# Performance work log

Hardware: AMD Instinct MI355X
Metric: run time of the kernel (lower is better)

Reference implementation:

```python
import jax, jax.numpy as jnp
import numpy as np

CH = 32          # channels
HID = CH * 16    # GRU hidden/input size = 512


def setup_inputs() -> dict:
    key = jax.random.key(0)
    ks = jax.random.split(key, 9)
    B, T = 512, 128
    s = 1.0 / np.sqrt(HID)
    frames = jax.random.uniform(ks[0], (B, T, 1, 16, 16), dtype=jnp.float32)
    conv_w = jax.random.normal(ks[1], (CH, 2, 4, 4), jnp.float32) * 0.1
    conv_b = jax.random.normal(ks[2], (CH,), jnp.float32) * 0.01
    w_ih = jax.random.uniform(ks[3], (3 * HID, HID), jnp.float32, -s, s)
    w_hh = jax.random.uniform(ks[4], (3 * HID, HID), jnp.float32, -s, s)
    b_ih = jax.random.uniform(ks[5], (3 * HID,), jnp.float32, -s, s)
    b_hh = jax.random.uniform(ks[6], (3 * HID,), jnp.float32, -s, s)
    deconv_w = jax.random.normal(ks[7], (CH, 1, 4, 4), jnp.float32) * 0.1
    deconv_b = jax.random.normal(ks[8], (1,), jnp.float32) * 0.01
    return {"frames": frames, "conv_w": conv_w, "conv_b": conv_b,
            "w_ih": w_ih, "w_hh": w_hh, "b_ih": b_ih, "b_hh": b_hh,
            "deconv_w": deconv_w, "deconv_b": deconv_b}


def reference(frames, conv_w, conv_b, w_ih, w_hh, b_ih, b_hh, deconv_w, deconv_b):
    B, T = frames.shape[0], frames.shape[1]
    T2 = T - 2
    curr = frames[:, 1:T - 1]              # (B,T2,1,16,16)
    prev = frames[:, :T - 2]               # (B,T2,1,16,16)
    diff = jnp.concatenate([curr, prev], axis=2)  # (B,T2,2,16,16)

    # Encoder: Conv2d(2,CH,4,stride=4). Stride==kernel -> non-overlapping patches.
    # Reshape HxW=16x16 into (i,p,j,q) with H=4i+p, W=4j+q.
    x = diff.reshape(B * T2, 2, 4, 4, 4, 4)                 # (n,c,i,p,j,q)
    enc = jnp.einsum('bcipjq,ocpq->boij', x, conv_w) + conv_b[None, :, None, None]
    feat = jax.nn.gelu(enc, approximate=False).reshape(B, T2, HID)  # flatten(1), exact GELU

    # GRU (single layer, batch_first, zero init hidden)
    gates_x = jnp.einsum('bti,gi->tbg', feat, w_ih) + b_ih  # (T2,B,3H)

    def step(h, gx):
        gh = h @ w_hh.T + b_hh
        gxr, gxz, gxn = jnp.split(gx, 3, axis=-1)
        ghr, ghz, ghn = jnp.split(gh, 3, axis=-1)
        r = jax.nn.sigmoid(gxr + ghr)
        z = jax.nn.sigmoid(gxz + ghz)
        n = jnp.tanh(gxn + r * ghn)
        h_new = (1.0 - z) * n + z * h
        return h_new, h_new

    h0 = jnp.zeros((B, HID), frames.dtype)
    _, outs = jax.lax.scan(step, h0, gates_x)               # (T2,B,HID)

    # Decoder: ConvTranspose2d(CH,1,4,stride=4). Stride==kernel -> scatter patches.
    dec_in = outs.transpose(1, 0, 2).reshape(B * T2, CH, 4, 4)
    dec = jnp.einsum('ncij,copq->noipjq', dec_in, deconv_w).reshape(B * T2, 1, 16, 16)
    delta = jnp.tanh(dec + deconv_b[None, :, None, None])

    pred = jnp.clip(curr.reshape(B * T2, 1, 16, 16) + delta, 0.0, 1.0)
    return pred.reshape(B, T2, 1, 16, 16)
```

## Files before the change

kernel.cpp:

```cpp
#include <hip/hip_runtime.h>
#include <cstdint>

typedef float f32x4 __attribute__((ext_vector_type(4)));
typedef __bf16 bf16x8 __attribute__((ext_vector_type(8)));
typedef unsigned short us8 __attribute__((ext_vector_type(8)));
typedef unsigned int u32x4 __attribute__((ext_vector_type(4)));

#define T2 126

__device__ __forceinline__ unsigned short f2bf(float x){
  union { float f; uint32_t u; } v; v.f = x;
  return (unsigned short)((v.u + 0x7fffu + ((v.u >> 16) & 1u)) >> 16);
}
__device__ __forceinline__ float bf2f(unsigned short h){
  union { uint32_t u; float f; } v; v.u = ((uint32_t)h) << 16; return v.f;
}
__device__ __forceinline__ f32x4 mfma_bf16(us8 a, us8 b, f32x4 c){
  return __builtin_amdgcn_mfma_f32_16x16x32_bf16(
      __builtin_bit_cast(bf16x8, a), __builtin_bit_cast(bf16x8, b), c, 0, 0, 0);
}
__device__ __forceinline__ float sigm(float x){ return 1.0f / (1.0f + __expf(-x)); }

#define HSWZ(row, chunk) ((row) * 512 + ((((chunk) ^ ((row) & 7))) << 3))

__global__ void __launch_bounds__(256) pack_w_kernel(const float* __restrict__ w,
                                                     unsigned short* __restrict__ dst){
  int tid = blockIdx.x * 256 + threadIdx.x;
  int l = tid & 63;
  int tile = tid >> 6;
  int kt = tile & 15, jt = tile >> 4;
  int row = jt * 16 + (l & 15);
  int col = kt * 32 + (l >> 4) * 8;
  const float* s = w + (size_t)row * 512 + col;
  unsigned short o[8];
  #pragma unroll
  for (int e = 0; e < 8; e++) o[e] = f2bf(s[e]);
  *(us8*)(dst + (size_t)tid * 8) = *(const us8*)o;
}

__global__ void __launch_bounds__(256) conv_gelu_kernel(const float* __restrict__ frames,
                                                        const float* __restrict__ cw,
                                                        const float* __restrict__ cb,
                                                        unsigned short* __restrict__ featg){
  __shared__ float im[512];
  __shared__ float wl[1024];
  int n = blockIdx.x;
  int t = n >> 9, b = n & 511;
  const float* fr = frames + ((size_t)b * 128 + t) * 256;
  int tid = threadIdx.x;
  ((float2*)im)[tid] = ((const float2*)fr)[tid];
  #pragma unroll
  for (int i = 0; i < 4; i++) wl[tid + 256 * i] = cw[tid + 256 * i];
  __syncthreads();
  #pragma unroll
  for (int half = 0; half < 2; half++){
    int oi = tid + half * 256;
    int o = oi >> 4, ii = (oi >> 2) & 3, jj = oi & 3;
    const float* wc = &wl[o * 32];
    float s = cb[o];
    #pragma unroll
    for (int p = 0; p < 4; p++)
      #pragma unroll
      for (int q = 0; q < 4; q++){
        int pix = (ii * 4 + p) * 16 + jj * 4 + q;
        s += im[256 + pix] * wc[p * 4 + q] + im[pix] * wc[16 + p * 4 + q];
      }
    float g = 0.5f * s * (1.0f + erff(s * 0.70710678118654752f));
    featg[(size_t)n * 512 + oi] = f2bf(g);
  }
}

__global__ void __launch_bounds__(256) scan_init_kernel(u32x4* __restrict__ hq,
                                                        unsigned int* __restrict__ tagbuf){
  int tid = blockIdx.x * 256 + threadIdx.x;
  int stride = gridDim.x * 256;
  for (int i = tid; i < 32768; i += stride)
    hq[i] = (u32x4){0u, 0u, 0u, 0u};
  for (int i = tid; i < 2 * 8 * 32 * 16; i += stride)
    tagbuf[i] = 0u;
}

__global__ void __launch_bounds__(256, 1) gru_scan_kernel(
    const unsigned short* __restrict__ whh_p,
    const unsigned short* __restrict__ wih_p,
    const float* __restrict__ b_hh,
    const float* __restrict__ b_ih,
    u32x4* __restrict__ hq,
    unsigned int* __restrict__ tagbuf,
    const unsigned short* __restrict__ featg,
    const float* __restrict__ frames,
    const float* __restrict__ dw,
    const float* __restrict__ db,
    float* __restrict__ out){
  __shared__ unsigned short hlds[16 * 512];
  __shared__ unsigned short featl[16 * 512];
  __shared__ unsigned short gbuf[2][3 * 16 * 72];
  __shared__ unsigned short hout[16 * 64];
  __shared__ float dwl[512];
  const int tid = threadIdx.x;
  const int B = blockIdx.x;
  const int grp = B & 31;
  const int slc = B >> 5;
  const int l = tid & 63;
  const int w = tid >> 6;
  const int lr = l & 15, lh = l >> 4;
  const int j = slc * 64 + w * 16 + lr;
  const int rowb = grp * 16;
  const int rloc = lh * 4;

  dwl[tid] = dw[tid]; dwl[tid + 256] = dw[tid + 256];
  const float dbias = db[0];

  us8 wr[16], wz[16], wn[16];
  {
    const int jt = slc * 4 + w;
    #pragma unroll
    for (int kt = 0; kt < 16; kt++){
      wr[kt] = *(volatile const us8*)(whh_p + ((size_t)((jt      ) * 16 + kt) * 512 + l * 8));
      wz[kt] = *(volatile const us8*)(whh_p + ((size_t)((jt + 32) * 16 + kt) * 512 + l * 8));
      wn[kt] = *(volatile const us8*)(whh_p + ((size_t)((jt + 64) * 16 + kt) * 512 + l * 8));
    }
  }
  const float bhr = b_hh[j], bhz = b_hh[512 + j], bhn = b_hh[1024 + j];

  int jtg[3], gg[3], wtt[3]; float gbias[3];
  #pragma unroll
  for (int jj = 0; jj < 3; jj++){
    int q = w * 3 + jj; gg[jj] = q >> 2; wtt[jj] = q & 3;
    jtg[jj] = gg[jj] * 32 + slc * 4 + wtt[jj];
    gbias[jj] = b_ih[gg[jj] * 512 + slc * 64 + wtt[jj] * 16 + lr];
  }
  float hprev[4] = {0.0f, 0.0f, 0.0f, 0.0f};
  __syncthreads();

  auto stagefeat = [&](int u){
    const u32x4* rb = (const u32x4*)(featg + (size_t)u * 512 * 512);
    int quad = tid & 63, r0 = tid >> 6;
    const u32x4* p0 = rb + ((size_t)(rowb + r0) * 64 + quad);
    u32x4 q0 = p0[0];
    u32x4 q1 = p0[4 * 64];
    u32x4 q2 = p0[8 * 64];
    u32x4 q3 = p0[12 * 64];
    *(u32x4*)&featl[HSWZ(r0,      quad)] = q0;
    *(u32x4*)&featl[HSWZ(r0 + 4,  quad)] = q1;
    *(u32x4*)&featl[HSWZ(r0 + 8,  quad)] = q2;
    *(u32x4*)&featl[HSWZ(r0 + 12, quad)] = q3;
    __syncthreads();
  };

  auto gatesgemm = [&](int par){
    f32x4 a0 = {0.f,0.f,0.f,0.f}, a1 = {0.f,0.f,0.f,0.f}, a2 = {0.f,0.f,0.f,0.f};
    #pragma unroll
    for (int kt = 0; kt < 16; kt++){
      us8 a = *(const us8*)&featl[HSWZ(lr, kt * 4 + lh)];
      us8 b0 = *(const us8*)(wih_p + ((size_t)(jtg[0] * 16 + kt) * 512 + l * 8));
      us8 b1 = *(const us8*)(wih_p + ((size_t)(jtg[1] * 16 + kt) * 512 + l * 8));
      us8 b2 = *(const us8*)(wih_p + ((size_t)(jtg[2] * 16 + kt) * 512 + l * 8));
      a0 = mfma_bf16(a, b0, a0);
      a1 = mfma_bf16(a, b1, a1);
      a2 = mfma_bf16(a, b2, a2);
    }
    unsigned short* gb = &gbuf[par][0];
    #pragma unroll
    for (int r = 0; r < 4; r++){
      gb[(gg[0] * 16 + lh * 4 + r) * 72 + wtt[0] * 16 + lr] = f2bf(a0[r] + gbias[0]);
      gb[(gg[1] * 16 + lh * 4 + r) * 72 + wtt[1] * 16 + lr] = f2bf(a1[r] + gbias[1]);
      gb[(gg[2] * 16 + lh * 4 + r) * 72 + wtt[2] * 16 + lr] = f2bf(a2[r] + gbias[2]);
    }
  };

  auto poll = [&](int s){
    if (tid < 8){
      const unsigned int* tp = tagbuf + (((size_t)(s & 1) * 8 + tid) * 32 + grp) * 16;
      unsigned int want = (unsigned)s;
      unsigned int tv;
      for (;;){
        asm volatile("global_load_dword %0, %1, off sc0 sc1\n\ts_waitcnt vmcnt(0)"
                     : "=&v"(tv) : "v"(tp) : "memory");
        if (tv >= want) break;
        __builtin_amdgcn_s_sleep(1);
      }
    }
    __syncthreads();
  };

  auto stage = [&](int s){
    const u32x4* rb = hq + (size_t)(s & 1) * 32768;
    int quad = tid & 63, r0 = tid >> 6;
    const u32x4* p0 = rb + ((size_t)(rowb + r0) * 64 + quad);
    const u32x4* p1 = p0 + 4 * 64;
    const u32x4* p2 = p0 + 8 * 64;
    const u32x4* p3 = p0 + 12 * 64;
    u32x4 q0, q1, q2, q3;
    asm volatile(
      "global_load_dwordx4 %0, %4, off sc0 sc1\n\t"
      "global_load_dwordx4 %1, %5, off sc0 sc1\n\t"
      "global_load_dwordx4 %2, %6, off sc0 sc1\n\t"
      "global_load_dwordx4 %3, %7, off sc0 sc1\n\t"
      "s_waitcnt vmcnt(0)"
      : "=&v"(q0), "=&v"(q1), "=&v"(q2), "=&v"(q3)
      : "v"(p0), "v"(p1), "v"(p2), "v"(p3)
      : "memory");
    *(u32x4*)&hlds[HSWZ(r0,      quad)] = q0;
    *(u32x4*)&hlds[HSWZ(r0 + 4,  quad)] = q1;
    *(u32x4*)&hlds[HSWZ(r0 + 8,  quad)] = q2;
    *(u32x4*)&hlds[HSWZ(r0 + 12, quad)] = q3;
    __syncthreads();
  };

  auto emit = [&](int so){
    int row = tid >> 4;
    int b = rowb + row;
    const float* fr = frames + ((size_t)b * 128 + so + 1) * 256;
    float* ob = out + ((size_t)b * T2 + so) * 256;
    #pragma unroll
    for (int e = 0; e < 2; e++){
      int pi = (tid & 15) * 2 + e;
      int pr = slc * 2 + (pi >> 4), pc = pi & 15;
      int ii = pr >> 2, pp = pr & 3, jj2 = pc >> 2, qq = pc & 3;
      float acc = dbias;
      #pragma unroll
      for (int c = 0; c < 32; c++){
        int ch = c * 16 + ii * 4 + jj2;
        acc += bf2f(hlds[HSWZ(row, ch >> 3) + (ch & 7)]) * dwl[c * 16 + pp * 4 + qq];
      }
      float dlt = tanhf(acc);
      float rv = fr[pr * 16 + pc] + dlt;
      ob[pr * 16 + pc] = fminf(fmaxf(rv, 0.0f), 1.0f);
    }
  };

  stagefeat(0);
  gatesgemm(0);

  for (int s = 0; s < T2; s++){
    if (s + 1 < T2){
      __syncthreads();
      stagefeat(s + 1);
      gatesgemm((s + 1) & 1);
    }
    poll(s);
    stage(s);
    f32x4 aR = {0.f,0.f,0.f,0.f}, aZ = {0.f,0.f,0.f,0.f}, aN = {0.f,0.f,0.f,0.f};
    #pragma unroll
    for (int kt = 0; kt < 16; kt++){
      us8 a = *(const us8*)&hlds[HSWZ(lr, kt * 4 + lh)];
      aR = mfma_bf16(a, wr[kt], aR);
      aZ = mfma_bf16(a, wz[kt], aZ);
      aN = mfma_bf16(a, wn[kt], aN);
    }
    const unsigned short* gb = &gbuf[s & 1][0];
    #pragma unroll
    for (int r = 0; r < 4; r++){
      float gxr = bf2f(gb[(      rloc + r) * 72 + w * 16 + lr]);
      float gxz = bf2f(gb[(16 + rloc + r) * 72 + w * 16 + lr]);
      float gxn = bf2f(gb[(32 + rloc + r) * 72 + w * 16 + lr]);
      float rr = sigm(gxr + aR[r] + bhr);
      float zz = sigm(gxz + aZ[r] + bhz);
      float nn = tanhf(gxn + rr * (aN[r] + bhn));
      float hv = (1.0f - zz) * nn + zz * hprev[r];
      hprev[r] = hv;
      hout[(rloc + r) * 64 + w * 16 + lr] = f2bf(hv);
    }
    __syncthreads();
    if (tid < 128){
      int row = tid >> 3, q = tid & 7;
      u32x4 hv = *(const u32x4*)&hout[row * 64 + q * 8];
      u32x4* dst = hq + ((size_t)(((s + 1) & 1) * 512 + rowb + row) * 64 + slc * 8 + q);
      asm volatile("global_store_dwordx4 %0, %1, off sc0 sc1" :: "v"(dst), "v"(hv) : "memory");
    }
    asm volatile("s_waitcnt vmcnt(0)" ::: "memory");
    __syncthreads();
    if (tid == 0){
      unsigned int tg = (unsigned)(s + 1);
      unsigned int* tp = tagbuf + (((size_t)((s + 1) & 1) * 8 + slc) * 32 + grp) * 16;
      asm volatile("global_store_dword %0, %1, off sc0 sc1" :: "v"(tp), "v"(tg) : "memory");
    }
    if (s >= 1) emit(s - 1);
  }
  poll(T2);
  stage(T2);
  emit(T2 - 1);
}

extern "C" void kernel_launch(void* const* d_in, const int* in_sizes, int n_in,
                              void* d_out, int out_size, void* d_ws, size_t ws_size,
                              hipStream_t stream) {
  const float* frames   = (const float*)d_in[0];
  const float* conv_w   = (const float*)d_in[1];
  const float* conv_b   = (const float*)d_in[2];
  const float* w_ih     = (const float*)d_in[3];
  const float* w_hh     = (const float*)d_in[4];
  const float* b_ih     = (const float*)d_in[5];
  const float* b_hh     = (const float*)d_in[6];
  const float* deconv_w = (const float*)d_in[7];
  const float* deconv_b = (const float*)d_in[8];
  float* out = (float*)d_out;
  char* ws = (char*)d_ws;

  unsigned short* wih_p  = (unsigned short*)(ws);
  unsigned short* whh_p  = (unsigned short*)(ws + 1572864LL);
  u32x4*          hq     = (u32x4*)         (ws + 3145728LL);
  unsigned int*   tagbuf = (unsigned int*)  (ws + 4194304LL);
  unsigned short* featg  = (unsigned short*)(ws + 4227072LL);

  pack_w_kernel<<<384, 256, 0, stream>>>(w_ih, wih_p);
  pack_w_kernel<<<384, 256, 0, stream>>>(w_hh, whh_p);
  scan_init_kernel<<<64, 256, 0, stream>>>(hq, tagbuf);
  conv_gelu_kernel<<<126 * 512, 256, 0, stream>>>(frames, conv_w, conv_b, featg);
  gru_scan_kernel<<<256, 256, 0, stream>>>(whh_p, wih_p, b_hh, b_ih, hq, tagbuf,
                                           featg, frames, deconv_w, deconv_b, out);
}
```

Baseline: 1.010 ms.

## Move next-step feature staging and input GEMM off the recurrence critical path

Feature prefetch and the input-gate GEMM for step s+1 now run after the hidden state for step s is published, not before polling. The feature loads are issued alongside the h store, and a partial vmcnt wait orders the h store before the tag store. This lets the input-side work overlap other blocks' latency in the cross-block recurrence instead of delaying each poll. It relies on careful vmcnt accounting: the wait assumes only the four feature loads may still be outstanding.

Measured after the change: 993.2 us. About the same (-1.7%).

```diff
diff --git a/kernel.cpp b/kernel.cpp
--- a/kernel.cpp
+++ b/kernel.cpp
@@ -133,20 +133,7 @@
   float hprev[4] = {0.0f, 0.0f, 0.0f, 0.0f};
   __syncthreads();
 
-  auto stagefeat = [&](int u){
-    const u32x4* rb = (const u32x4*)(featg + (size_t)u * 512 * 512);
-    int quad = tid & 63, r0 = tid >> 6;
-    const u32x4* p0 = rb + ((size_t)(rowb + r0) * 64 + quad);
-    u32x4 q0 = p0[0];
-    u32x4 q1 = p0[4 * 64];
-    u32x4 q2 = p0[8 * 64];
-    u32x4 q3 = p0[12 * 64];
-    *(u32x4*)&featl[HSWZ(r0,      quad)] = q0;
-    *(u32x4*)&featl[HSWZ(r0 + 4,  quad)] = q1;
-    *(u32x4*)&featl[HSWZ(r0 + 8,  quad)] = q2;
-    *(u32x4*)&featl[HSWZ(r0 + 12, quad)] = q3;
-    __syncthreads();
-  };
+  const int fquad = tid & 63, fr0 = tid >> 6;
 
   auto gatesgemm = [&](int par){
     f32x4 a0 = {0.f,0.f,0.f,0.f}, a1 = {0.f,0.f,0.f,0.f}, a2 = {0.f,0.f,0.f,0.f};
@@ -186,8 +173,7 @@
 
   auto stage = [&](int s){
     const u32x4* rb = hq + (size_t)(s & 1) * 32768;
-    int quad = tid & 63, r0 = tid >> 6;
-    const u32x4* p0 = rb + ((size_t)(rowb + r0) * 64 + quad);
+    const u32x4* p0 = rb + ((size_t)(rowb + fr0) * 64 + fquad);
     const u32x4* p1 = p0 + 4 * 64;
     const u32x4* p2 = p0 + 8 * 64;
     const u32x4* p3 = p0 + 12 * 64;
@@ -201,10 +187,10 @@
       : "=&v"(q0), "=&v"(q1), "=&v"(q2), "=&v"(q3)
       : "v"(p0), "v"(p1), "v"(p2), "v"(p3)
       : "memory");
-    *(u32x4*)&hlds[HSWZ(r0,      quad)] = q0;
-    *(u32x4*)&hlds[HSWZ(r0 + 4,  quad)] = q1;
-    *(u32x4*)&hlds[HSWZ(r0 + 8,  quad)] = q2;
-    *(u32x4*)&hlds[HSWZ(r0 + 12, quad)] = q3;
+    *(u32x4*)&hlds[HSWZ(fr0,      fquad)] = q0;
+    *(u32x4*)&hlds[HSWZ(fr0 + 4,  fquad)] = q1;
+    *(u32x4*)&hlds[HSWZ(fr0 + 8,  fquad)] = q2;
+    *(u32x4*)&hlds[HSWZ(fr0 + 12, fquad)] = q3;
     __syncthreads();
   };
 
@@ -230,15 +216,19 @@
     }
   };
 
-  stagefeat(0);
-  gatesgemm(0);
+  {
+    const u32x4* rb = (const u32x4*)featg;
+    const u32x4* p0 = rb + ((size_t)(rowb + fr0) * 64 + fquad);
+    u32x4 q0 = p0[0], q1 = p0[4 * 64], q2 = p0[8 * 64], q3 = p0[12 * 64];
+    *(u32x4*)&featl[HSWZ(fr0,      fquad)] = q0;
+    *(u32x4*)&featl[HSWZ(fr0 + 4,  fquad)] = q1;
+    *(u32x4*)&featl[HSWZ(fr0 + 8,  fquad)] = q2;
+    *(u32x4*)&featl[HSWZ(fr0 + 12, fquad)] = q3;
+    __syncthreads();
+    gatesgemm(0);
+  }
 
   for (int s = 0; s < T2; s++){
-    if (s + 1 < T2){
-      __syncthreads();
-      stagefeat(s + 1);
-      gatesgemm((s + 1) & 1);
-    }
     poll(s);
     stage(s);
     f32x4 aR = {0.f,0.f,0.f,0.f}, aZ = {0.f,0.f,0.f,0.f}, aN = {0.f,0.f,0.f,0.f};
@@ -269,12 +259,41 @@
       u32x4* dst = hq + ((size_t)(((s + 1) & 1) * 512 + rowb + row) * 64 + slc * 8 + q);
       asm volatile("global_store_dwordx4 %0, %1, off sc0 sc1" :: "v"(dst), "v"(hv) : "memory");
     }
-    asm volatile("s_waitcnt vmcnt(0)" ::: "memory");
+    u32x4 f0, f1, f2, f3;
+    const bool more = (s + 1 < T2);
+    if (more){
+      const u32x4* rb = (const u32x4*)(featg + (size_t)(s + 1) * 512 * 512);
+      const u32x4* p0 = rb + ((size_t)(rowb + fr0) * 64 + fquad);
+      const u32x4* p1 = p0 + 4 * 64;
+      const u32x4* p2 = p0 + 8 * 64;
+      const u32x4* p3 = p0 + 12 * 64;
+      asm volatile(
+        "global_load_dwordx4 %0, %4, off\n\t"
+        "global_load_dwordx4 %1, %5, off\n\t"
+        "global_load_dwordx4 %2, %6, off\n\t"
+        "global_load_dwordx4 %3, %7, off"
+        : "=&v"(f0), "=&v"(f1), "=&v"(f2), "=&v"(f3)
+        : "v"(p0), "v"(p1), "v"(p2), "v"(p3)
+        : "memory");
+      asm volatile("s_waitcnt vmcnt(4)" ::: "memory");
+    } else {
+      asm volatile("s_waitcnt vmcnt(0)" ::: "memory");
+    }
     __syncthreads();
     if (tid == 0){
       unsigned int tg = (unsigned)(s + 1);
       unsigned int* tp = tagbuf + (((size_t)((s + 1) & 1) * 8 + slc) * 32 + grp) * 16;
       asm volatile("global_store_dword %0, %1, off sc0 sc1" :: "v"(tp), "v"(tg) : "memory");
+    }
+    if (more){
+      asm volatile("s_waitcnt vmcnt(0)" ::: "memory");
+      __builtin_amdgcn_sched_barrier(0);
+      *(u32x4*)&featl[HSWZ(fr0,      fquad)] = f0;
+      *(u32x4*)&featl[HSWZ(fr0 + 4,  fquad)] = f1;
+      *(u32x4*)&featl[HSWZ(fr0 + 8,  fquad)] = f2;
+      *(u32x4*)&featl[HSWZ(fr0 + 12, fquad)] = f3;
+      __syncthreads();
+      gatesgemm((s + 1) & 1);
     }
     if (s >= 1) emit(s - 1);
   }
```
